# Kernel optimization log

Hardware: AMD Instinct MI355X
Metric: run time of the kernel (lower is better)

The kernel has to match this reference:

```python
import jax, jax.numpy as jnp
import numpy as np

B, S, I, H, O = 64, 4096, 256, 256, 128


def setup_inputs() -> dict:
    key = jax.random.key(0)
    ks = jax.random.split(key, 7)
    s_in = 1.0 / np.sqrt(I)
    s_h = 1.0 / np.sqrt(H)
    return {
        "x": jax.random.normal(ks[0], (B, S, I), dtype=jnp.float32),
        "Wax_w": jax.random.uniform(ks[1], (H, I), jnp.float32, -s_in, s_in),
        "Wax_b": jax.random.uniform(ks[2], (H,), jnp.float32, -s_in, s_in),
        "Waa_w": jax.random.uniform(ks[3], (H, H), jnp.float32, -s_h, s_h),
        "Waa_b": jax.random.uniform(ks[4], (H,), jnp.float32, -s_h, s_h),
        "Wya_w": jax.random.uniform(ks[5], (O, H), jnp.float32, -s_h, s_h),
        "Wya_b": jax.random.uniform(ks[6], (O,), jnp.float32, -s_h, s_h),
    }


def reference(x, Wax_w, Wax_b, Waa_w, Waa_b, Wya_w, Wya_b):
    # Precompute input projections for all timesteps in one big GEMM: [B,S,H]
    xp = jnp.einsum("bsi,hi->bsh", x, Wax_w) + Wax_b

    def step(a_prev, xp_t):
        a_next = jnp.tanh(xp_t + a_prev @ Waa_w.T + Waa_b)
        return a_next, None

    a0 = jnp.zeros((x.shape[0], Waa_w.shape[0]), dtype=x.dtype)
    a_last, _ = jax.lax.scan(step, a0, jnp.swapaxes(xp, 0, 1))  # scan over S
    return jax.nn.sigmoid(a_last @ Wya_w.T + Wya_b)
```

## Files before the change

### kernel.cpp

```cpp
#include <hip/hip_runtime.h>
#include <hip/hip_fp16.h>


typedef _Float16 f16x8 __attribute__((ext_vector_type(8)));
typedef _Float16 f16x4 __attribute__((ext_vector_type(4)));
typedef _Float16 f16x2 __attribute__((ext_vector_type(2)));
typedef float    f32x4 __attribute__((ext_vector_type(4)));

#define FDOT2(a, b, c) __builtin_amdgcn_fdot2((a), (b), (c), false)

template <int D>
__device__ __forceinline__ float rorf(float v) {
    return __builtin_bit_cast(float,
        __builtin_amdgcn_update_dpp(0, __builtin_bit_cast(int, v),
                                    0x120 + D, 0xF, 0xF, true));
}

__global__ __launch_bounds__(512) void k_xp(
    const float* __restrict__ x, const float* __restrict__ Ww,
    const float* __restrict__ Wb, _Float16* __restrict__ xp,
    int c, int T_C, int logT)
{
    __shared__ __align__(16) _Float16 As[64 * 264];
    const int tid  = threadIdx.x;
    const int lane = tid & 63;
    const int wv   = tid >> 6;
    const int l15  = lane & 15;
    const int lk   = lane >> 4;
    const int n0   = wv * 32;

    f16x8 bfr[2][8];
#pragma unroll
    for (int nt = 0; nt < 2; ++nt) {
        const float* wrow = Ww + (size_t)(n0 + nt * 16 + l15) * 256;
#pragma unroll
        for (int kt = 0; kt < 8; ++kt) {
            const float4* wp = (const float4*)(wrow + kt * 32 + lk * 8);
            float4 v0 = wp[0], v1 = wp[1];
            f16x8 f;
            f[0] = (_Float16)v0.x; f[1] = (_Float16)v0.y;
            f[2] = (_Float16)v0.z; f[3] = (_Float16)v0.w;
            f[4] = (_Float16)v1.x; f[5] = (_Float16)v1.y;
            f[6] = (_Float16)v1.z; f[7] = (_Float16)v1.w;
            bfr[nt][kt] = f;
        }
    }
    const float bias0 = Wb[n0 + l15];
    const float bias1 = Wb[n0 + 16 + l15];

    {
        const int arow = tid >> 3;
        const int acol = (tid & 7) * 32;
        const int r    = blockIdx.x * 64 + arow;
        const int bb   = r >> logT;
        const int tl   = r & (T_C - 1);
        const float4* s4 = (const float4*)(x + ((size_t)(bb * 4096 + c * T_C + tl) << 8) + acol);
        _Float16* d = As + arow * 264 + acol;
#pragma unroll
        for (int q = 0; q < 4; ++q) {
            float4 v0 = s4[2 * q], v1 = s4[2 * q + 1];
            f16x8 p;
            p[0] = (_Float16)v0.x; p[1] = (_Float16)v0.y;
            p[2] = (_Float16)v0.z; p[3] = (_Float16)v0.w;
            p[4] = (_Float16)v1.x; p[5] = (_Float16)v1.y;
            p[6] = (_Float16)v1.z; p[7] = (_Float16)v1.w;
            *(f16x8*)(d + q * 8) = p;
        }
    }
    __syncthreads();

    f32x4 acc[4][2] = {};
#pragma unroll
    for (int kt = 0; kt < 8; ++kt) {
#pragma unroll
        for (int mt = 0; mt < 4; ++mt) {
            f16x8 af = *(const f16x8*)(As + (mt * 16 + l15) * 264 + kt * 32 + lk * 8);
            acc[mt][0] = __builtin_amdgcn_mfma_f32_16x16x32_f16(af, bfr[0][kt], acc[mt][0], 0, 0, 0);
            acc[mt][1] = __builtin_amdgcn_mfma_f32_16x16x32_f16(af, bfr[1][kt], acc[mt][1], 0, 0, 0);
        }
    }

    const int base = blockIdx.x * 64;
#pragma unroll
    for (int mt = 0; mt < 4; ++mt) {
        const int rr  = base + mt * 16 + lk * 4;
        const int bb2 = rr >> logT;
        const int tt  = rr & (T_C - 1);
#pragma unroll
        for (int nt = 0; nt < 2; ++nt) {
            const int   h    = n0 + nt * 16 + l15;
            const float bias = (nt == 0) ? bias0 : bias1;
            f16x4 pk;
#pragma unroll
            for (int r2 = 0; r2 < 4; ++r2) pk[r2] = (_Float16)(acc[mt][nt][r2] + bias);
            *(f16x4*)(xp + ((size_t)(bb2 * 256 + h)) * T_C + tt) = pk;
        }
    }
}

__global__ __launch_bounds__(1024, 4) void k_rnn(
    const _Float16* __restrict__ xp, const float* __restrict__ Waa,
    const float* __restrict__ Wab, const float* __restrict__ Wya,
    const float* __restrict__ Wyb, float* __restrict__ out,
    unsigned short* __restrict__ a_state,
    int c, int T_C, int is_last)
{
    __shared__ __align__(16) _Float16 aL[2][16][24];
    __shared__ float afin[256];
    const int tid   = threadIdx.x;
    const int lane  = tid & 63;
    const int w     = tid >> 6;
    const int k     = lane & 15;
    const int g     = lane >> 4;
    const int rbase = w * 16 + g * 4;
    const int myrow = rbase + (k & 3);
    const int b     = blockIdx.x;
    const bool wlane = (k & 12) == 0;

    f16x2 wr[4][8];
#pragma unroll
    for (int i = 0; i < 4; ++i) {
        const float4* wp = (const float4*)(Waa + (size_t)(rbase + ((k + i) & 3)) * 256 + k * 16);
#pragma unroll
        for (int q = 0; q < 4; ++q) {
            float4 v = wp[q];
            f16x2 t0; t0[0] = (_Float16)v.x; t0[1] = (_Float16)v.y;
            f16x2 t1; t1[0] = (_Float16)v.z; t1[1] = (_Float16)v.w;
            wr[i][2 * q]     = t0;
            wr[i][2 * q + 1] = t1;
        }
    }
    const float bias = Wab[myrow];

    if (tid < 256) {
        unsigned short v = 0;
        if (c != 0) v = a_state[b * 256 + tid];
        aL[0][tid >> 4][tid & 15] = __builtin_bit_cast(_Float16, v);
    }
    __syncthreads();

    const _Float16* xph = xp + ((size_t)(b * 256 + myrow)) * T_C;
    f16x8 xq = *(const f16x8*)(xph);
    float bx[8];
#pragma unroll
    for (int j = 0; j < 8; ++j) bx[j] = bias + (float)xq[j];

    const _Float16* rp0 = &aL[0][k][0];
    const _Float16* rp1 = &aL[1][k][0];
    _Float16* wq0 = &aL[1][w][g * 4 + k];
    _Float16* wq1 = &aL[0][w][g * 4 + k];

#define RNN_STEP(J, FIN)                                                     \
    {                                                                        \
        const _Float16* rp = ((J) & 1) ? rp1 : rp0;                          \
        uint4 r0 = *(const uint4*)(rp);                                      \
        uint4 r1 = *(const uint4*)(rp + 8);                                  \
        f16x2 a2[8];                                                         \
        a2[0] = __builtin_bit_cast(f16x2, r0.x);                             \
        a2[1] = __builtin_bit_cast(f16x2, r0.y);                             \
        a2[2] = __builtin_bit_cast(f16x2, r0.z);                             \
        a2[3] = __builtin_bit_cast(f16x2, r0.w);                             \
        a2[4] = __builtin_bit_cast(f16x2, r1.x);                             \
        a2[5] = __builtin_bit_cast(f16x2, r1.y);                             \
        a2[6] = __builtin_bit_cast(f16x2, r1.z);                             \
        a2[7] = __builtin_bit_cast(f16x2, r1.w);                             \
        float s0 = 0.f, s1 = 0.f, s2 = 0.f, s3 = 0.f;                        \
        _Pragma("unroll")                                                    \
        for (int q = 0; q < 8; ++q) {                                        \
            s0 = FDOT2(wr[0][q], a2[q], s0);                                 \
            s1 = FDOT2(wr[1][q], a2[q], s1);                                 \
            s2 = FDOT2(wr[2][q], a2[q], s2);                                 \
            s3 = FDOT2(wr[3][q], a2[q], s3);                                 \
        }                                                                    \
        float p0 = s0 + rorf<8>(s0);                                         \
        float p1 = s1 + rorf<8>(s1);                                         \
        float p2 = s2 + rorf<8>(s2);                                         \
        float p3 = s3 + rorf<8>(s3);                                         \
        float q0 = p0 + rorf<4>(p0);                                         \
        float q1 = p1 + rorf<4>(p1);                                         \
        float q2 = p2 + rorf<4>(p2);                                         \
        float q3 = p3 + rorf<4>(p3);                                         \
        float acc = (q0 + rorf<1>(q1)) + (rorf<2>(q2) + rorf<3>(q3));        \
        float z  = bx[(J)] + acc;                                            \
        float e2 = __expf(2.f * z);                                          \
        float a  = fmaf(-2.f, __builtin_amdgcn_rcpf(e2 + 1.f), 1.f);         \
        _Float16 ah = (_Float16)a;                                           \
        if (wlane) *(((J) & 1) ? wq1 : wq0) = ah;                            \
        if (FIN) {                                                           \
            afin[myrow] = a;                                                 \
            a_state[b * 256 + myrow] = __builtin_bit_cast(unsigned short, ah);\
        }                                                                    \
        asm volatile("s_waitcnt lgkmcnt(0)" ::: "memory");                   \
        __builtin_amdgcn_s_barrier();                                        \
        asm volatile("" ::: "memory");                                       \
    }

    for (int tb = 0; tb + 8 < T_C; tb += 8) {
        f16x8 xn = *(const f16x8*)(xph + tb + 8);
        RNN_STEP(0, false) RNN_STEP(1, false) RNN_STEP(2, false) RNN_STEP(3, false)
        RNN_STEP(4, false) RNN_STEP(5, false) RNN_STEP(6, false) RNN_STEP(7, false)
#pragma unroll
        for (int j = 0; j < 8; ++j) bx[j] = bias + (float)xn[j];
    }
    RNN_STEP(0, false) RNN_STEP(1, false) RNN_STEP(2, false) RNN_STEP(3, false)
    RNN_STEP(4, false) RNN_STEP(5, false) RNN_STEP(6, false) RNN_STEP(7, true)
#undef RNN_STEP

    if (is_last) {
        const int o  = tid >> 3;
        const int k8 = tid & 7;
        const float4* wp = (const float4*)(Wya + (size_t)o * 256 + k8 * 32);
        const float4* ap = (const float4*)(afin + k8 * 32);
        float s = 0.f;
#pragma unroll
        for (int i = 0; i < 8; ++i) {
            float4 wv4 = wp[i];
            float4 a4  = ap[i];
            s += wv4.x * a4.x + wv4.y * a4.y + wv4.z * a4.z + wv4.w * a4.w;
        }
        s += __shfl_xor(s, 1);
        s += __shfl_xor(s, 2);
        s += __shfl_xor(s, 4);
        if (k8 == 0)
            out[b * 128 + o] = __builtin_amdgcn_rcpf(1.f + __expf(-(s + Wyb[o])));
    }
}

extern "C" void kernel_launch(void* const* d_in, const int* in_sizes, int n_in,
                              void* d_out, int out_size, void* d_ws, size_t ws_size,
                              hipStream_t stream)
{
    (void)in_sizes; (void)n_in; (void)out_size;
    const float* x    = (const float*)d_in[0];
    const float* Waxw = (const float*)d_in[1];
    const float* Waxb = (const float*)d_in[2];
    const float* Waaw = (const float*)d_in[3];
    const float* Waab = (const float*)d_in[4];
    const float* Wyaw = (const float*)d_in[5];
    const float* Wyab = (const float*)d_in[6];
    float* out = (float*)d_out;

    int T_C = 4096, logT = 12;
    while (T_C > 32 && (size_t)64 * T_C * 256 * 2 + 32768 > ws_size) { T_C >>= 1; --logT; }

    _Float16* xp = (_Float16*)d_ws;
    unsigned short* a_state =
        (unsigned short*)((char*)d_ws + (size_t)64 * T_C * 256 * 2);

    const int nc = 4096 / T_C;
    for (int ci = 0; ci < nc; ++ci) {
        k_xp<<<dim3(T_C), dim3(512), 0, stream>>>(x, Waxw, Waxb, xp, ci, T_C, logT);
        k_rnn<<<dim3(64), dim3(1024), 0, stream>>>(xp, Waaw, Waab, Wyaw, Wyab,
                                                   out, a_state, ci, T_C, ci == nc - 1);
    }
}
```

Baseline: 2.240 ms.

## Fuse projection GEMM and recurrence into one kernel with double-buffered chunk pipelining

Merges the input-projection GEMM and the recurrent scan into a single launch. The first 64 blocks run the recurrence on chunk i-1 while the remaining blocks compute projections for chunk i into a second xp buffer, so the serial scan overlaps with the memory-bound GEMM. Chunk size is fixed at 1024, and GEMM blocks now cover 128 rows with 16 waves. The cross-lane reduction is also reordered to rotate within quads first, which uses fewer DPP ops. The risk is that the GEMM blocks compete with the latency-bound scan blocks for CU resources, and the larger shared allocation sits in every block.

```diff
diff --git a/kernel.cpp b/kernel.cpp
--- a/kernel.cpp
+++ b/kernel.cpp
@@ -15,140 +15,74 @@
         __builtin_amdgcn_update_dpp(0, __builtin_bit_cast(int, v),
                                     0x120 + D, 0xF, 0xF, true));
 }
-
-__global__ __launch_bounds__(512) void k_xp(
+template <int D>
+__device__ __forceinline__ float qrot(float v) {
+    constexpr int ctrl = D == 1 ? 0x93 : (D == 2 ? 0x4E : 0x39);
+    return __builtin_bit_cast(float,
+        __builtin_amdgcn_update_dpp(0, __builtin_bit_cast(int, v),
+                                    ctrl, 0xF, 0xF, true));
+}
+
+__global__ __launch_bounds__(1024) void k_fused(
     const float* __restrict__ x, const float* __restrict__ Ww,
-    const float* __restrict__ Wb, _Float16* __restrict__ xp,
-    int c, int T_C, int logT)
+    const float* __restrict__ Wb, const float* __restrict__ Waa,
+    const float* __restrict__ Wab, const float* __restrict__ Wya,
+    const float* __restrict__ Wyb, float* __restrict__ out,
+    _Float16* __restrict__ xp0, _Float16* __restrict__ xp1,
+    unsigned short* __restrict__ a_state,
+    int c_rnn, int c_xp, int do_rnn, int do_xp, int is_last,
+    int T_C, int logT)
 {
-    __shared__ __align__(16) _Float16 As[64 * 264];
+    __shared__ __align__(16) _Float16 As[128 * 264];
+    __shared__ __align__(16) _Float16 aL[2][16][24];
+    __shared__ float afin[256];
+
     const int tid  = threadIdx.x;
     const int lane = tid & 63;
-    const int wv   = tid >> 6;
-    const int l15  = lane & 15;
-    const int lk   = lane >> 4;
-    const int n0   = wv * 32;
-
-    f16x8 bfr[2][8];
-#pragma unroll
-    for (int nt = 0; nt < 2; ++nt) {
-        const float* wrow = Ww + (size_t)(n0 + nt * 16 + l15) * 256;
-#pragma unroll
-        for (int kt = 0; kt < 8; ++kt) {
-            const float4* wp = (const float4*)(wrow + kt * 32 + lk * 8);
-            float4 v0 = wp[0], v1 = wp[1];
-            f16x8 f;
-            f[0] = (_Float16)v0.x; f[1] = (_Float16)v0.y;
-            f[2] = (_Float16)v0.z; f[3] = (_Float16)v0.w;
-            f[4] = (_Float16)v1.x; f[5] = (_Float16)v1.y;
-            f[6] = (_Float16)v1.z; f[7] = (_Float16)v1.w;
-            bfr[nt][kt] = f;
-        }
-    }
-    const float bias0 = Wb[n0 + l15];
-    const float bias1 = Wb[n0 + 16 + l15];
-
-    {
-        const int arow = tid >> 3;
-        const int acol = (tid & 7) * 32;
-        const int r    = blockIdx.x * 64 + arow;
-        const int bb   = r >> logT;
-        const int tl   = r & (T_C - 1);
-        const float4* s4 = (const float4*)(x + ((size_t)(bb * 4096 + c * T_C + tl) << 8) + acol);
-        _Float16* d = As + arow * 264 + acol;
-#pragma unroll
-        for (int q = 0; q < 4; ++q) {
-            float4 v0 = s4[2 * q], v1 = s4[2 * q + 1];
-            f16x8 p;
-            p[0] = (_Float16)v0.x; p[1] = (_Float16)v0.y;
-            p[2] = (_Float16)v0.z; p[3] = (_Float16)v0.w;
-            p[4] = (_Float16)v1.x; p[5] = (_Float16)v1.y;
-            p[6] = (_Float16)v1.z; p[7] = (_Float16)v1.w;
-            *(f16x8*)(d + q * 8) = p;
-        }
-    }
-    __syncthreads();
-
-    f32x4 acc[4][2] = {};
-#pragma unroll
-    for (int kt = 0; kt < 8; ++kt) {
-#pragma unroll
-        for (int mt = 0; mt < 4; ++mt) {
-            f16x8 af = *(const f16x8*)(As + (mt * 16 + l15) * 264 + kt * 32 + lk * 8);
-            acc[mt][0] = __builtin_amdgcn_mfma_f32_16x16x32_f16(af, bfr[0][kt], acc[mt][0], 0, 0, 0);
-            acc[mt][1] = __builtin_amdgcn_mfma_f32_16x16x32_f16(af, bfr[1][kt], acc[mt][1], 0, 0, 0);
-        }
-    }
-
-    const int base = blockIdx.x * 64;
-#pragma unroll
-    for (int mt = 0; mt < 4; ++mt) {
-        const int rr  = base + mt * 16 + lk * 4;
-        const int bb2 = rr >> logT;
-        const int tt  = rr & (T_C - 1);
-#pragma unroll
-        for (int nt = 0; nt < 2; ++nt) {
-            const int   h    = n0 + nt * 16 + l15;
-            const float bias = (nt == 0) ? bias0 : bias1;
-            f16x4 pk;
-#pragma unroll
-            for (int r2 = 0; r2 < 4; ++r2) pk[r2] = (_Float16)(acc[mt][nt][r2] + bias);
-            *(f16x4*)(xp + ((size_t)(bb2 * 256 + h)) * T_C + tt) = pk;
-        }
-    }
-}
-
-__global__ __launch_bounds__(1024, 4) void k_rnn(
-    const _Float16* __restrict__ xp, const float* __restrict__ Waa,
-    const float* __restrict__ Wab, const float* __restrict__ Wya,
-    const float* __restrict__ Wyb, float* __restrict__ out,
-    unsigned short* __restrict__ a_state,
-    int c, int T_C, int is_last)
-{
-    __shared__ __align__(16) _Float16 aL[2][16][24];
-    __shared__ float afin[256];
-    const int tid   = threadIdx.x;
-    const int lane  = tid & 63;
-    const int w     = tid >> 6;
-    const int k     = lane & 15;
-    const int g     = lane >> 4;
-    const int rbase = w * 16 + g * 4;
-    const int myrow = rbase + (k & 3);
-    const int b     = blockIdx.x;
-    const bool wlane = (k & 12) == 0;
-
-    f16x2 wr[4][8];
-#pragma unroll
-    for (int i = 0; i < 4; ++i) {
-        const float4* wp = (const float4*)(Waa + (size_t)(rbase + ((k + i) & 3)) * 256 + k * 16);
-#pragma unroll
-        for (int q = 0; q < 4; ++q) {
-            float4 v = wp[q];
-            f16x2 t0; t0[0] = (_Float16)v.x; t0[1] = (_Float16)v.y;
-            f16x2 t1; t1[0] = (_Float16)v.z; t1[1] = (_Float16)v.w;
-            wr[i][2 * q]     = t0;
-            wr[i][2 * q + 1] = t1;
-        }
-    }
-    const float bias = Wab[myrow];
-
-    if (tid < 256) {
-        unsigned short v = 0;
-        if (c != 0) v = a_state[b * 256 + tid];
-        aL[0][tid >> 4][tid & 15] = __builtin_bit_cast(_Float16, v);
-    }
-    __syncthreads();
-
-    const _Float16* xph = xp + ((size_t)(b * 256 + myrow)) * T_C;
-    f16x8 xq = *(const f16x8*)(xph);
-    float bx[8];
-#pragma unroll
-    for (int j = 0; j < 8; ++j) bx[j] = bias + (float)xq[j];
-
-    const _Float16* rp0 = &aL[0][k][0];
-    const _Float16* rp1 = &aL[1][k][0];
-    _Float16* wq0 = &aL[1][w][g * 4 + k];
-    _Float16* wq1 = &aL[0][w][g * 4 + k];
+
+    if (blockIdx.x < 64) {
+        if (!do_rnn) return;
+        const _Float16* xp = (c_rnn & 1) ? xp1 : xp0;
+        const int w     = tid >> 6;
+        const int k     = lane & 15;
+        const int g     = lane >> 4;
+        const int rbase = w * 16 + g * 4;
+        const int myrow = rbase + (k & 3);
+        const int b     = blockIdx.x;
+        const bool wlane = (k & 12) == 0;
+
+        f16x2 wr[4][8];
+#pragma unroll
+        for (int i = 0; i < 4; ++i) {
+            const float4* wp = (const float4*)(Waa + (size_t)(rbase + ((k + i) & 3)) * 256 + k * 16);
+#pragma unroll
+            for (int q = 0; q < 4; ++q) {
+                float4 v = wp[q];
+                f16x2 t0; t0[0] = (_Float16)v.x; t0[1] = (_Float16)v.y;
+                f16x2 t1; t1[0] = (_Float16)v.z; t1[1] = (_Float16)v.w;
+                wr[i][2 * q]     = t0;
+                wr[i][2 * q + 1] = t1;
+            }
+        }
+        const float bias = Wab[myrow];
+
+        if (tid < 256) {
+            unsigned short v = 0;
+            if (c_rnn != 0) v = a_state[b * 256 + tid];
+            aL[0][tid >> 4][tid & 15] = __builtin_bit_cast(_Float16, v);
+        }
+        __syncthreads();
+
+        const _Float16* xph = xp + ((size_t)(b * 256 + myrow)) * T_C;
+        f16x8 xq = *(const f16x8*)(xph);
+        float bx[8];
+#pragma unroll
+        for (int j = 0; j < 8; ++j) bx[j] = bias + (float)xq[j];
+
+        const _Float16* rp0 = &aL[0][k][0];
+        const _Float16* rp1 = &aL[1][k][0];
+        _Float16* wq0 = &aL[1][w][g * 4 + k];
+        _Float16* wq1 = &aL[0][w][g * 4 + k];
 
 #define RNN_STEP(J, FIN)                                                     \
     {                                                                        \
@@ -172,15 +106,12 @@
             s2 = FDOT2(wr[2][q], a2[q], s2);                                 \
             s3 = FDOT2(wr[3][q], a2[q], s3);                                 \
         }                                                                    \
-        float p0 = s0 + rorf<8>(s0);                                         \
-        float p1 = s1 + rorf<8>(s1);                                         \
-        float p2 = s2 + rorf<8>(s2);                                         \
-        float p3 = s3 + rorf<8>(s3);                                         \
-        float q0 = p0 + rorf<4>(p0);                                         \
-        float q1 = p1 + rorf<4>(p1);                                         \
-        float q2 = p2 + rorf<4>(p2);                                         \
-        float q3 = p3 + rorf<4>(p3);                                         \
-        float acc = (q0 + rorf<1>(q1)) + (rorf<2>(q2) + rorf<3>(q3));        \
+                 \
+        float t = s0 + qrot<1>(s1);                                          \
+        t += qrot<2>(s2);                                                    \
+        t += qrot<3>(s3);                                                    \
+        float u   = t + rorf<4>(t);                                          \
+        float acc = u + rorf<8>(u);                                          \
         float z  = bx[(J)] + acc;                                            \
         float e2 = __expf(2.f * z);                                          \
         float a  = fmaf(-2.f, __builtin_amdgcn_rcpf(e2 + 1.f), 1.f);         \
@@ -195,34 +126,103 @@
         asm volatile("" ::: "memory");                                       \
     }
 
-    for (int tb = 0; tb + 8 < T_C; tb += 8) {
-        f16x8 xn = *(const f16x8*)(xph + tb + 8);
+        for (int tb = 0; tb + 8 < T_C; tb += 8) {
+            f16x8 xn = *(const f16x8*)(xph + tb + 8);
+            RNN_STEP(0, false) RNN_STEP(1, false) RNN_STEP(2, false) RNN_STEP(3, false)
+            RNN_STEP(4, false) RNN_STEP(5, false) RNN_STEP(6, false) RNN_STEP(7, false)
+#pragma unroll
+            for (int j = 0; j < 8; ++j) bx[j] = bias + (float)xn[j];
+        }
         RNN_STEP(0, false) RNN_STEP(1, false) RNN_STEP(2, false) RNN_STEP(3, false)
-        RNN_STEP(4, false) RNN_STEP(5, false) RNN_STEP(6, false) RNN_STEP(7, false)
-#pragma unroll
-        for (int j = 0; j < 8; ++j) bx[j] = bias + (float)xn[j];
-    }
-    RNN_STEP(0, false) RNN_STEP(1, false) RNN_STEP(2, false) RNN_STEP(3, false)
-    RNN_STEP(4, false) RNN_STEP(5, false) RNN_STEP(6, false) RNN_STEP(7, true)
+        RNN_STEP(4, false) RNN_STEP(5, false) RNN_STEP(6, false) RNN_STEP(7, true)
 #undef RNN_STEP
 
-    if (is_last) {
-        const int o  = tid >> 3;
-        const int k8 = tid & 7;
-        const float4* wp = (const float4*)(Wya + (size_t)o * 256 + k8 * 32);
-        const float4* ap = (const float4*)(afin + k8 * 32);
-        float s = 0.f;
-#pragma unroll
-        for (int i = 0; i < 8; ++i) {
-            float4 wv4 = wp[i];
-            float4 a4  = ap[i];
-            s += wv4.x * a4.x + wv4.y * a4.y + wv4.z * a4.z + wv4.w * a4.w;
-        }
-        s += __shfl_xor(s, 1);
-        s += __shfl_xor(s, 2);
-        s += __shfl_xor(s, 4);
-        if (k8 == 0)
-            out[b * 128 + o] = __builtin_amdgcn_rcpf(1.f + __expf(-(s + Wyb[o])));
+        if (is_last) {
+            const int o  = tid >> 3;
+            const int k8 = tid & 7;
+            const float4* wp = (const float4*)(Wya + (size_t)o * 256 + k8 * 32);
+            const float4* ap = (const float4*)(afin + k8 * 32);
+            float s = 0.f;
+#pragma unroll
+            for (int i = 0; i < 8; ++i) {
+                float4 wv4 = wp[i];
+                float4 a4  = ap[i];
+                s += wv4.x * a4.x + wv4.y * a4.y + wv4.z * a4.z + wv4.w * a4.w;
+            }
+            s += __shfl_xor(s, 1);
+            s += __shfl_xor(s, 2);
+            s += __shfl_xor(s, 4);
+            if (k8 == 0)
+                out[b * 128 + o] = __builtin_amdgcn_rcpf(1.f + __expf(-(s + Wyb[o])));
+        }
+    } else {
+        if (!do_xp) return;
+        _Float16* xp = (c_xp & 1) ? xp1 : xp0;
+        const int bxp = blockIdx.x - 64;
+        const int wv  = tid >> 6;
+        const int l15 = lane & 15;
+        const int lk  = lane >> 4;
+        const int n0  = wv * 16;
+
+        f16x8 bfr[8];
+        {
+            const float* wrow = Ww + (size_t)(n0 + l15) * 256;
+#pragma unroll
+            for (int kt = 0; kt < 8; ++kt) {
+                const float4* wp = (const float4*)(wrow + kt * 32 + lk * 8);
+                float4 v0 = wp[0], v1 = wp[1];
+                f16x8 f;
+                f[0] = (_Float16)v0.x; f[1] = (_Float16)v0.y;
+                f[2] = (_Float16)v0.z; f[3] = (_Float16)v0.w;
+                f[4] = (_Float16)v1.x; f[5] = (_Float16)v1.y;
+                f[6] = (_Float16)v1.z; f[7] = (_Float16)v1.w;
+                bfr[kt] = f;
+            }
+        }
+        const float bias = Wb[n0 + l15];
+
+        {
+            const int arow = tid >> 3;
+            const int acol = (tid & 7) * 32;
+            const int r    = bxp * 128 + arow;
+            const int bb   = r >> logT;
+            const int tl   = r & (T_C - 1);
+            const float4* s4 = (const float4*)(x + ((size_t)(bb * 4096 + c_xp * T_C + tl) << 8) + acol);
+            _Float16* d = As + arow * 264 + acol;
+#pragma unroll
+            for (int q = 0; q < 4; ++q) {
+                float4 v0 = s4[2 * q], v1 = s4[2 * q + 1];
+                f16x8 p;
+                p[0] = (_Float16)v0.x; p[1] = (_Float16)v0.y;
+                p[2] = (_Float16)v0.z; p[3] = (_Float16)v0.w;
+                p[4] = (_Float16)v1.x; p[5] = (_Float16)v1.y;
+                p[6] = (_Float16)v1.z; p[7] = (_Float16)v1.w;
+                *(f16x8*)(d + q * 8) = p;
+            }
+        }
+        __syncthreads();
+
+        f32x4 acc[8] = {};
+#pragma unroll
+        for (int kt = 0; kt < 8; ++kt) {
+#pragma unroll
+            for (int mt = 0; mt < 8; ++mt) {
+                f16x8 af = *(const f16x8*)(As + (mt * 16 + l15) * 264 + kt * 32 + lk * 8);
+                acc[mt] = __builtin_amdgcn_mfma_f32_16x16x32_f16(af, bfr[kt], acc[mt], 0, 0, 0);
+            }
+        }
+
+        const int base = bxp * 128;
+#pragma unroll
+        for (int mt = 0; mt < 8; ++mt) {
+            const int rr  = base + mt * 16 + lk * 4;
+            const int bb2 = rr >> logT;
+            const int tt  = rr & (T_C - 1);
+            f16x4 pk;
+#pragma unroll
+            for (int r2 = 0; r2 < 4; ++r2) pk[r2] = (_Float16)(acc[mt][r2] + bias);
+            *(f16x4*)(xp + ((size_t)(bb2 * 256 + n0 + l15)) * T_C + tt) = pk;
+        }
     }
 }
 
@@ -240,17 +240,19 @@
     const float* Wyab = (const float*)d_in[6];
     float* out = (float*)d_out;
 
-    int T_C = 4096, logT = 12;
-    while (T_C > 32 && (size_t)64 * T_C * 256 * 2 + 32768 > ws_size) { T_C >>= 1; --logT; }
-
-    _Float16* xp = (_Float16*)d_ws;
-    unsigned short* a_state =
-        (unsigned short*)((char*)d_ws + (size_t)64 * T_C * 256 * 2);
-
-    const int nc = 4096 / T_C;
-    for (int ci = 0; ci < nc; ++ci) {
-        k_xp<<<dim3(T_C), dim3(512), 0, stream>>>(x, Waxw, Waxb, xp, ci, T_C, logT);
-        k_rnn<<<dim3(64), dim3(1024), 0, stream>>>(xp, Waaw, Waab, Wyaw, Wyab,
-                                                   out, a_state, ci, T_C, ci == nc - 1);
+    int T_C = 1024, logT = 10;
+    while (T_C > 128 && (size_t)2 * 64 * T_C * 256 * 2 + 32768 > ws_size) { T_C >>= 1; --logT; }
+
+    _Float16* xp0 = (_Float16*)d_ws;
+    _Float16* xp1 = xp0 + (size_t)64 * T_C * 256;
+    unsigned short* a_state = (unsigned short*)(xp1 + (size_t)64 * T_C * 256);
+
+    const int nc  = 4096 / T_C;
+    const int nxp = 64 * T_C / 128;
+    for (int i = 0; i <= nc; ++i) {
+        k_fused<<<dim3(64 + nxp), dim3(1024), 0, stream>>>(
+            x, Waxw, Waxb, Waaw, Waab, Wyaw, Wyab, out, xp0, xp1, a_state,
+            i - 1, i, i >= 1 ? 1 : 0, i < nc ? 1 : 0, i == nc ? 1 : 0,
+            T_C, logT);
     }
 }
```

New measurement: 1.958 ms. 12.6% less time.
